# Optimization experiments

Measured on AMD Instinct MI355X. Metric: run time of the kernel, lower is better.

## Reference

```python
import jax, jax.numpy as jnp
import numpy as np

N = 100_000
E = 1_250_000
D = 64
PAIRS = 3  # layer_num=3 -> 3 (SAGE, GIN) pairs
EPS = 1e-5


def _linear_init(key, fi, fo):
    lim = 1.0 / np.sqrt(fi)
    k1, k2 = jax.random.split(key)
    W = jax.random.uniform(k1, (fi, fo), minval=-lim, maxval=lim, dtype=jnp.float32)
    b = jax.random.uniform(k2, (fo,), minval=-lim, maxval=lim, dtype=jnp.float32)
    return W, b


def setup_inputs() -> dict:
    key = jax.random.key(0)
    ks = jax.random.split(key, 40)
    # graph
    src = jax.random.randint(ks[0], (E,), 0, N, dtype=jnp.int32)
    dst = jax.random.randint(ks[1], (E,), 0, N, dtype=jnp.int32)
    sign = (jax.random.randint(ks[2], (E,), 0, 2, dtype=jnp.int32) * 2 - 1)
    edge_index_s = jnp.stack([src, dst, sign], axis=1)  # [E,3]
    init_emb = jax.random.normal(ks[3], (N, D), dtype=jnp.float32)
    rate_b = jax.random.uniform(ks[4], (1,), dtype=jnp.float32)

    def stack_lin(kbase, fi, fo, n):
        Ws, bs = [], []
        for i in range(n):
            W, b = _linear_init(jax.random.fold_in(kbase, i), fi, fo)
            Ws.append(W); bs.append(b)
        return jnp.stack(Ws), jnp.stack(bs)

    sage_lin_W, sage_lin_b = stack_lin(ks[5], D, D, PAIRS)
    sage_norm_w = jnp.ones((PAIRS, D), jnp.float32)
    sage_norm_b = jnp.zeros((PAIRS, D), jnp.float32)
    rsW, rsB = stack_lin(ks[6], 1, D, PAIRS)   # rate_scale Linear(1,D)
    rbW, rbB = stack_lin(ks[7], 1, D, PAIRS)   # rate_bias Linear(1,D)
    sage_rs_w, sage_rs_b = rsW[:, 0, :], rsB   # [PAIRS,D]
    sage_rb_w, sage_rb_b = rbW[:, 0, :], rbB
    gin_W1, gin_b1 = stack_lin(ks[8], D, D, PAIRS)
    gin_W2, gin_b2 = stack_lin(ks[9], D, D, PAIRS)
    fuse_W, fuse_b = _linear_init(ks[10], 2 * PAIRS * D, D)
    ro_W1, ro_b1 = _linear_init(ks[11], D, 128)
    ro_W2, ro_b2 = _linear_init(ks[12], 128, 128)
    ro_W3, ro_b3 = _linear_init(ks[13], 128, 1)
    ro_ln1_g = jnp.ones((128,), jnp.float32); ro_ln1_b = jnp.zeros((128,), jnp.float32)
    ro_ln2_g = jnp.ones((128,), jnp.float32); ro_ln2_b = jnp.zeros((128,), jnp.float32)
    return dict(init_emb=init_emb, edge_index_s=edge_index_s, rate_b=rate_b,
                sage_lin_W=sage_lin_W, sage_lin_b=sage_lin_b,
                sage_norm_w=sage_norm_w, sage_norm_b=sage_norm_b,
                sage_rs_w=sage_rs_w, sage_rs_b=sage_rs_b,
                sage_rb_w=sage_rb_w, sage_rb_b=sage_rb_b,
                gin_W1=gin_W1, gin_b1=gin_b1, gin_W2=gin_W2, gin_b2=gin_b2,
                fuse_W=fuse_W, fuse_b=fuse_b,
                ro_W1=ro_W1, ro_b1=ro_b1, ro_ln1_g=ro_ln1_g, ro_ln1_b=ro_ln1_b,
                ro_W2=ro_W2, ro_b2=ro_b2, ro_ln2_g=ro_ln2_g, ro_ln2_b=ro_ln2_b,
                ro_W3=ro_W3, ro_b3=ro_b3)


def _graph_norm(x, w, b, rs_w, rs_b, rb_w, rb_b, rate):
    # batch stats over nodes (dim 0), biased variance
    mean = x.mean(0, keepdims=True)
    var = x.var(0, keepdims=True)
    x_norm = (x - mean) / jnp.sqrt(var + EPS)
    gamma = w + (rs_w * rate + rs_b)  # rate_scale(rate_b)
    beta = b + (rb_w * rate + rb_b)
    return x_norm * gamma + beta


def _layer_norm(v, g, b):
    m = v.mean(-1, keepdims=True)
    va = v.var(-1, keepdims=True)
    return (v - m) / jnp.sqrt(va + EPS) * g + b


def _forward(init_emb, edge_index_s, rate_b,
             sage_lin_W, sage_lin_b, sage_norm_w, sage_norm_b,
             sage_rs_w, sage_rs_b, sage_rb_w, sage_rb_b,
             gin_W1, gin_b1, gin_W2, gin_b2,
             fuse_W, fuse_b,
             ro_W1, ro_b1, ro_ln1_g, ro_ln1_b,
             ro_W2, ro_b2, ro_ln2_g, ro_ln2_b,
             ro_W3, ro_b3):
    n = init_emb.shape[0]
    src = edge_index_s[:, 0]
    dst = edge_index_s[:, 1]
    sign = edge_index_s[:, 2].astype(init_emb.dtype)
    rate = rate_b.reshape(())
    # degree including self-loop (for mean aggregation with fill_value=1 self loops)
    deg = jax.ops.segment_sum(jnp.ones_like(sign), dst, num_segments=n) + 1.0  # [n]
    gelu = lambda t: jax.nn.gelu(t, approximate=False)  # torch nn.GELU default = exact

    x = init_emb
    outputs = []
    for i in range(PAIRS):
        # --- StableEfficientEdgeSAGEConv (mean aggr, sign-scaled, self-loops, skip=Identity) ---
        xt = x @ sage_lin_W[i] + sage_lin_b[i]
        msg = sign[:, None] * xt[src]                                   # gather + sign scale
        agg = (jax.ops.segment_sum(msg, dst, num_segments=n) + xt) / deg[:, None]
        h = agg + x                                                     # skip (in==out -> Identity)
        h = _graph_norm(h, sage_norm_w[i], sage_norm_b[i],
                        sage_rs_w[i], sage_rs_b[i], sage_rb_w[i], sage_rb_b[i], rate)
        x = gelu(h)                                                     # dropout: eval mode (no-op)
        outputs.append(x)
        # --- GINConv (sum aggr, eps=0, no self-loops) mlp = Lin-GELU-Lin ---
        agg2 = jax.ops.segment_sum(x[src], dst, num_segments=n)
        z = x + agg2
        x = gelu(z @ gin_W1[i] + gin_b1[i]) @ gin_W2[i] + gin_b2[i]
        outputs.append(x)

    x_dense = jnp.concatenate(outputs, axis=1)          # [n, 6*D]
    x_final = x_dense @ fuse_W + fuse_b                 # [n, D]
    # readout MLP (2 hidden layers + head), eval-mode dropout
    hdd = jax.nn.relu(_layer_norm(x_final @ ro_W1 + ro_b1, ro_ln1_g, ro_ln1_b))
    hdd = jax.nn.relu(_layer_norm(hdd @ ro_W2 + ro_b2, ro_ln2_g, ro_ln2_b))
    prob = jax.nn.sigmoid(hdd @ ro_W3 + ro_b3)          # [n, 1]
    return x_final, prob


def reference(init_emb, edge_index_s, rate_b,
              sage_lin_W, sage_lin_b, sage_norm_w, sage_norm_b,
              sage_rs_w, sage_rs_b, sage_rb_w, sage_rb_b,
              gin_W1, gin_b1, gin_W2, gin_b2,
              fuse_W, fuse_b,
              ro_W1, ro_b1, ro_ln1_g, ro_ln1_b,
              ro_W2, ro_b2, ro_ln2_g, ro_ln2_b,
              ro_W3, ro_b3):
    return _forward(init_emb, edge_index_s, rate_b,
                    sage_lin_W, sage_lin_b, sage_norm_w, sage_norm_b,
                    sage_rs_w, sage_rs_b, sage_rb_w, sage_rb_b,
                    gin_W1, gin_b1, gin_W2, gin_b2,
                    fuse_W, fuse_b,
                    ro_W1, ro_b1, ro_ln1_g, ro_ln1_b,
                    ro_W2, ro_b2, ro_ln2_g, ro_ln2_b,
                    ro_W3, ro_b3)
```

## Files before the change

kernel.cpp:

```cpp
#include <hip/hip_runtime.h>
#include <hip/hip_bf16.h>
#include <math.h>


#define NBSHIFT 9
#define NBSIZE  512

__device__ __forceinline__ float gelu_f(float x) {
    return 0.5f * x * (1.0f + erff(x * 0.70710678118654752440f));
}
__device__ __forceinline__ unsigned short f2bf(float x) {
    __hip_bfloat16 h = __float2bfloat16(x);
    return *reinterpret_cast<unsigned short*>(&h);
}
__device__ __forceinline__ unsigned pack2bf(float a, float b) {
    return (unsigned)f2bf(a) | ((unsigned)f2bf(b) << 16);
}
__device__ __forceinline__ float bf2f(unsigned short u) {
    return __uint_as_float((unsigned)u << 16);
}

__global__ __launch_bounds__(256) void gemm64(
    const float* __restrict__ A,
    const float* __restrict__ Wa, const float* __restrict__ ba,
    unsigned short* __restrict__ Cb, int n)
{
    __shared__ __align__(16) float At[64][68];
    __shared__ __align__(16) float Ws[64][68];
    const int tid = threadIdx.x;
    const int tx = tid & 15, ty = tid >> 4;
    const int rowBase = blockIdx.x * 64;

    #pragma unroll
    for (int i = 0; i < 4; ++i) {
        int v  = tid + i * 256;
        int r  = v >> 4;
        int k4 = (v & 15) * 4;
        float4 a = make_float4(0.f, 0.f, 0.f, 0.f);
        int grow = rowBase + r;
        if (grow < n) a = *(const float4*)(A + (size_t)grow * 64 + k4);
        At[k4 + 0][r] = a.x; At[k4 + 1][r] = a.y;
        At[k4 + 2][r] = a.z; At[k4 + 3][r] = a.w;
        *(float4*)&Ws[r][k4] = *(const float4*)(Wa + r * 64 + k4);
    }
    __syncthreads();

    const int r0 = ty * 4, c0 = tx * 4;
    float acc[4][4];
    #pragma unroll
    for (int j = 0; j < 4; ++j) {
        float bv = ba[c0 + j];
        #pragma unroll
        for (int i = 0; i < 4; ++i) acc[i][j] = bv;
    }
    #pragma unroll 16
    for (int k = 0; k < 64; ++k) {
        float4 av = *(const float4*)&At[k][r0];
        float4 wv = *(const float4*)&Ws[k][c0];
        float a4[4] = {av.x, av.y, av.z, av.w};
        float w4[4] = {wv.x, wv.y, wv.z, wv.w};
        #pragma unroll
        for (int i = 0; i < 4; ++i)
            #pragma unroll
            for (int j = 0; j < 4; ++j)
                acc[i][j] = fmaf(a4[i], w4[j], acc[i][j]);
    }
    #pragma unroll
    for (int i = 0; i < 4; ++i) {
        int grow = rowBase + r0 + i;
        if (grow < n) {
            uint2 u;
            u.x = pack2bf(acc[i][0], acc[i][1]);
            u.y = pack2bf(acc[i][2], acc[i][3]);
            *(uint2*)(Cb + (size_t)grow * 64 + c0) = u;
        }
    }
}

template<bool FIRST>
__global__ __launch_bounds__(256) void act_fuse(
    const float* __restrict__ h,
    const float* __restrict__ colsum, const float* __restrict__ colsumsq,
    const float* __restrict__ nw, const float* __restrict__ nb,
    const float* __restrict__ rsw, const float* __restrict__ rsb,
    const float* __restrict__ rbw, const float* __restrict__ rbb,
    const float* __restrict__ rate_p, float inv_n,
    const float* __restrict__ Wf, const float* __restrict__ bf,
    unsigned short* __restrict__ xb, float* __restrict__ xfinal, int n)
{
    __shared__ __align__(16) float At[64][68];
    __shared__ __align__(16) float Ws[64][68];
    __shared__ float ab_s[128];
    const int tid = threadIdx.x;
    const int tx = tid & 15, ty = tid >> 4;
    const int rowBase = blockIdx.x * 64;

    if (tid < 64) {
        float mean = colsum[tid] * inv_n;
        float var  = colsumsq[tid] * inv_n - mean * mean;
        float rstd = rsqrtf(var + 1e-5f);
        float rate = rate_p[0];
        float gamma = nw[tid] + (rsw[tid] * rate + rsb[tid]);
        float beta  = nb[tid] + (rbw[tid] * rate + rbb[tid]);
        float a = rstd * gamma;
        ab_s[tid] = a;
        ab_s[64 + tid] = beta - mean * a;
    }
    __syncthreads();

    #pragma unroll
    for (int i = 0; i < 4; ++i) {
        int v  = tid + i * 256;
        int r  = v >> 4;
        int k4 = (v & 15) * 4;
        int grow = rowBase + r;
        float4 a = make_float4(0.f, 0.f, 0.f, 0.f);
        if (grow < n) {
            float4 hv = *(const float4*)(h + (size_t)grow * 64 + k4);
            a.x = gelu_f(fmaf(hv.x, ab_s[k4 + 0], ab_s[64 + k4 + 0]));
            a.y = gelu_f(fmaf(hv.y, ab_s[k4 + 1], ab_s[64 + k4 + 1]));
            a.z = gelu_f(fmaf(hv.z, ab_s[k4 + 2], ab_s[64 + k4 + 2]));
            a.w = gelu_f(fmaf(hv.w, ab_s[k4 + 3], ab_s[64 + k4 + 3]));
            uint2 u;
            u.x = pack2bf(a.x, a.y);
            u.y = pack2bf(a.z, a.w);
            *(uint2*)(xb + (size_t)grow * 64 + k4) = u;
        }
        At[k4 + 0][r] = a.x; At[k4 + 1][r] = a.y;
        At[k4 + 2][r] = a.z; At[k4 + 3][r] = a.w;
        *(float4*)&Ws[r][k4] = *(const float4*)(Wf + r * 64 + k4);
    }
    __syncthreads();

    const int r0 = ty * 4, c0 = tx * 4;
    float acc[4][4];
    if (FIRST) {
        #pragma unroll
        for (int j = 0; j < 4; ++j) {
            float bv = bf[c0 + j];
            #pragma unroll
            for (int i = 0; i < 4; ++i) acc[i][j] = bv;
        }
    } else {
        #pragma unroll
        for (int i = 0; i < 4; ++i)
            #pragma unroll
            for (int j = 0; j < 4; ++j) acc[i][j] = 0.f;
    }
    #pragma unroll 16
    for (int k = 0; k < 64; ++k) {
        float4 av = *(const float4*)&At[k][r0];
        float4 wv = *(const float4*)&Ws[k][c0];
        float a4[4] = {av.x, av.y, av.z, av.w};
        float w4[4] = {wv.x, wv.y, wv.z, wv.w};
        #pragma unroll
        for (int i = 0; i < 4; ++i)
            #pragma unroll
            for (int j = 0; j < 4; ++j)
                acc[i][j] = fmaf(a4[i], w4[j], acc[i][j]);
    }
    #pragma unroll
    for (int i = 0; i < 4; ++i) {
        int grow = rowBase + r0 + i;
        if (grow < n) {
            float4 r = make_float4(acc[i][0], acc[i][1], acc[i][2], acc[i][3]);
            float* cp = xfinal + (size_t)grow * 64 + c0;
            if (!FIRST) {
                float4 c = *(const float4*)cp;
                r.x += c.x; r.y += c.y; r.z += c.z; r.w += c.w;
            }
            *(float4*)cp = r;
        }
    }
}

template<bool NEXT>
__global__ __launch_bounds__(256) void gin_fuse(
    const float* __restrict__ z,
    const float* __restrict__ W1, const float* __restrict__ b1,
    const float* __restrict__ W2, const float* __restrict__ b2,
    const float* __restrict__ Wf,
    const float* __restrict__ Wn, const float* __restrict__ bn,
    float* __restrict__ xout, float* __restrict__ xfinal,
    unsigned short* __restrict__ bfout, int n)
{
    __shared__ __align__(16) float At[64][68];
    __shared__ __align__(16) float Ws[64][68];
    const int tid = threadIdx.x;
    const int tx = tid & 15, ty = tid >> 4;
    const int rowBase = blockIdx.x * 64;
    const int r0 = ty * 4, c0 = tx * 4;

    #pragma unroll
    for (int i = 0; i < 4; ++i) {
        int v  = tid + i * 256;
        int r  = v >> 4;
        int k4 = (v & 15) * 4;
        float4 a = make_float4(0.f, 0.f, 0.f, 0.f);
        int grow = rowBase + r;
        if (grow < n) a = *(const float4*)(z + (size_t)grow * 64 + k4);
        At[k4 + 0][r] = a.x; At[k4 + 1][r] = a.y;
        At[k4 + 2][r] = a.z; At[k4 + 3][r] = a.w;
        *(float4*)&Ws[r][k4] = *(const float4*)(W1 + r * 64 + k4);
    }
    __syncthreads();

    float acc[4][4];
    #pragma unroll
    for (int j = 0; j < 4; ++j) {
        float bv = b1[c0 + j];
        #pragma unroll
        for (int i = 0; i < 4; ++i) acc[i][j] = bv;
    }
    #pragma unroll 16
    for (int k = 0; k < 64; ++k) {
        float4 av = *(const float4*)&At[k][r0];
        float4 wv = *(const float4*)&Ws[k][c0];
        float a4[4] = {av.x, av.y, av.z, av.w};
        float w4[4] = {wv.x, wv.y, wv.z, wv.w};
        #pragma unroll
        for (int i = 0; i < 4; ++i)
            #pragma unroll
            for (int j = 0; j < 4; ++j)
                acc[i][j] = fmaf(a4[i], w4[j], acc[i][j]);
    }

    __syncthreads();
    #pragma unroll
    for (int i = 0; i < 4; ++i)
        #pragma unroll
        for (int j = 0; j < 4; ++j)
            At[c0 + j][r0 + i] = gelu_f(acc[i][j]);
    #pragma unroll
    for (int i = 0; i < 4; ++i) {
        int v = tid + i * 256;
        int k = v >> 4, c4 = (v & 15) * 4;
        *(float4*)&Ws[k][c4] = *(const float4*)(W2 + k * 64 + c4);
    }
    __syncthreads();
    float acc2[4][4];
    #pragma unroll
    for (int j = 0; j < 4; ++j) {
        float bv = b2[c0 + j];
        #pragma unroll
        for (int i = 0; i < 4; ++i) acc2[i][j] = bv;
    }
    #pragma unroll 16
    for (int k = 0; k < 64; ++k) {
        float4 av = *(const float4*)&At[k][r0];
        float4 wv = *(const float4*)&Ws[k][c0];
        float a4[4] = {av.x, av.y, av.z, av.w};
        float w4[4] = {wv.x, wv.y, wv.z, wv.w};
        #pragma unroll
        for (int i = 0; i < 4; ++i)
            #pragma unroll
            for (int j = 0; j < 4; ++j)
                acc2[i][j] = fmaf(a4[i], w4[j], acc2[i][j]);
    }
    #pragma unroll
    for (int i = 0; i < 4; ++i) {
        int grow = rowBase + r0 + i;
        if (grow < n)
            *(float4*)(xout + (size_t)grow * 64 + c0) =
                make_float4(acc2[i][0], acc2[i][1], acc2[i][2], acc2[i][3]);
    }

    __syncthreads();
    #pragma unroll
    for (int i = 0; i < 4; ++i)
        #pragma unroll
        for (int j = 0; j < 4; ++j)
            At[c0 + j][r0 + i] = acc2[i][j];
    #pragma unroll
    for (int i = 0; i < 4; ++i) {
        int v = tid + i * 256;
        int k = v >> 4, c4 = (v & 15) * 4;
        *(float4*)&Ws[k][c4] = *(const float4*)(Wf + k * 64 + c4);
    }
    __syncthreads();
    float acc3[4][4];
    #pragma unroll
    for (int i = 0; i < 4; ++i)
        #pragma unroll
        for (int j = 0; j < 4; ++j) acc3[i][j] = 0.f;
    #pragma unroll 16
    for (int k = 0; k < 64; ++k) {
        float4 av = *(const float4*)&At[k][r0];
        float4 wv = *(const float4*)&Ws[k][c0];
        float a4[4] = {av.x, av.y, av.z, av.w};
        float w4[4] = {wv.x, wv.y, wv.z, wv.w};
        #pragma unroll
        for (int i = 0; i < 4; ++i)
            #pragma unroll
            for (int j = 0; j < 4; ++j)
                acc3[i][j] = fmaf(a4[i], w4[j], acc3[i][j]);
    }
    #pragma unroll
    for (int i = 0; i < 4; ++i) {
        int grow = rowBase + r0 + i;
        if (grow < n) {
            float* cp = xfinal + (size_t)grow * 64 + c0;
            float4 c = *(const float4*)cp;
            c.x += acc3[i][0]; c.y += acc3[i][1];
            c.z += acc3[i][2]; c.w += acc3[i][3];
            *(float4*)cp = c;
        }
    }

    if (NEXT) {
        __syncthreads();
        #pragma unroll
        for (int i = 0; i < 4; ++i) {
            int v = tid + i * 256;
            int k = v >> 4, c4 = (v & 15) * 4;
            *(float4*)&Ws[k][c4] = *(const float4*)(Wn + k * 64 + c4);
        }
        __syncthreads();
        float acc4[4][4];
        #pragma unroll
        for (int j = 0; j < 4; ++j) {
            float bv = bn[c0 + j];
            #pragma unroll
            for (int i = 0; i < 4; ++i) acc4[i][j] = bv;
        }
        #pragma unroll 16
        for (int k = 0; k < 64; ++k) {
            float4 av = *(const float4*)&At[k][r0];
            float4 wv = *(const float4*)&Ws[k][c0];
            float a4[4] = {av.x, av.y, av.z, av.w};
            float w4[4] = {wv.x, wv.y, wv.z, wv.w};
            #pragma unroll
            for (int i = 0; i < 4; ++i)
                #pragma unroll
                for (int j = 0; j < 4; ++j)
                    acc4[i][j] = fmaf(a4[i], w4[j], acc4[i][j]);
        }
        #pragma unroll
        for (int i = 0; i < 4; ++i) {
            int grow = rowBase + r0 + i;
            if (grow < n) {
                uint2 u;
                u.x = pack2bf(acc4[i][0], acc4[i][1]);
                u.y = pack2bf(acc4[i][2], acc4[i][3]);
                *(uint2*)(bfout + (size_t)grow * 64 + c0) = u;
            }
        }
    }
}

__global__ void init_buckets(int* __restrict__ bucket_cursor, int Bn, int cap) {
    int t = threadIdx.x;
    if (t < Bn) bucket_cursor[t] = t * cap;
}

__global__ __launch_bounds__(256) void bucketA(
    const int* __restrict__ eidx, int* __restrict__ bucket_cursor,
    uint2* __restrict__ inter, int E)
{
    __shared__ int cnt[256], lo[256], cur[256], garr[256];
    __shared__ int tot_s;
    __shared__ uint2 stage[4096];
    const int tid = threadIdx.x;
    cnt[tid] = 0;
    __syncthreads();

    const int base = blockIdx.x * 4096;
    int pay[16], dfull[16];
    #pragma unroll
    for (int i = 0; i < 16; ++i) {
        int e = base + i * 256 + tid;
        dfull[i] = -1;
        if (e < E) {
            int s  = __builtin_nontemporal_load(eidx + e * 3 + 0);
            int d  = __builtin_nontemporal_load(eidx + e * 3 + 1);
            int sg = __builtin_nontemporal_load(eidx + e * 3 + 2);
            if (sg < 0) s |= 0x80000000;
            pay[i] = s;
            dfull[i] = d;
            atomicAdd(&cnt[d >> NBSHIFT], 1);
        }
    }
    __syncthreads();

    lo[tid] = cnt[tid];
    __syncthreads();
    for (int off = 1; off < 256; off <<= 1) {
        int t = (tid >= off) ? lo[tid - off] : 0;
        __syncthreads();
        lo[tid] += t;
        __syncthreads();
    }
    if (tid == 255) tot_s = lo[255];
    int excl = lo[tid] - cnt[tid];
    __syncthreads();
    lo[tid] = excl;
    cur[tid] = 0;
    if (cnt[tid] > 0) garr[tid] = atomicAdd(bucket_cursor + tid, cnt[tid]);
    __syncthreads();

    #pragma unroll
    for (int i = 0; i < 16; ++i) {
        if (dfull[i] >= 0) {
            int k = dfull[i] >> NBSHIFT;
            int r = atomicAdd(&cur[k], 1);
            stage[lo[k] + r] = make_uint2((unsigned)pay[i], (unsigned)dfull[i]);
        }
    }
    __syncthreads();

    const int tot = tot_s;
    for (int i = tid; i < tot; i += 256) {
        uint2 en = stage[i];
        int k = (int)(en.y >> NBSHIFT);
        inter[garr[k] + (i - lo[k])] = en;
    }
}

__global__ __launch_bounds__(256) void bucketB1(
    const uint2* __restrict__ inter, const int* __restrict__ bucket_cursor,
    int* __restrict__ deg_i, int cap, int n)
{
    __shared__ int cnt[NBSIZE];
    const int b = blockIdx.x, tid = threadIdx.x;
    cnt[tid] = 0; cnt[tid + 256] = 0;
    __syncthreads();
    const int base = b * cap;
    const int len = bucket_cursor[b] - base;
    for (int i = tid; i < len; i += 256)
        atomicAdd(&cnt[inter[base + i].y & (NBSIZE - 1)], 1);
    __syncthreads();
    const int nb0 = b << NBSHIFT;
    if (nb0 + tid < n)       deg_i[nb0 + tid]       = cnt[tid];
    if (nb0 + 256 + tid < n) deg_i[nb0 + 256 + tid] = cnt[256 + tid];
}

__global__ __launch_bounds__(256) void bucketB2(
    const uint2* __restrict__ inter, const int* __restrict__ bucket_cursor,
    const int* __restrict__ row_ptr, int* __restrict__ payload, int cap, int n)
{
    __shared__ int cur[NBSIZE];
    const int b = blockIdx.x, tid = threadIdx.x;
    const int nb0 = b << NBSHIFT;
    cur[tid]       = (nb0 + tid < n)       ? row_ptr[nb0 + tid]       : 0;
    cur[tid + 256] = (nb0 + 256 + tid < n) ? row_ptr[nb0 + 256 + tid] : 0;
    __syncthreads();
    const int base = b * cap;
    const int len = bucket_cursor[b] - base;
    for (int i = tid; i < len; i += 256) {
        uint2 en = inter[base + i];
        int pos = atomicAdd(&cur[en.y & (NBSIZE - 1)], 1);
        payload[pos] = (int)en.x;
    }
}

__global__ __launch_bounds__(256) void scan1(
    const int* __restrict__ deg_i, int* __restrict__ blocksum, int n, int chunk)
{
    int b = blockIdx.x;
    int lo = b * chunk, hi = min(lo + chunk, n);
    int s = 0;
    for (int i = lo + (int)threadIdx.x; i < hi; i += 256) s += deg_i[i];
    #pragma unroll
    for (int off = 32; off; off >>= 1) s += __shfl_xor(s, off, 64);
    __shared__ int ws[4];
    if ((threadIdx.x & 63) == 0) ws[threadIdx.x >> 6] = s;
    __syncthreads();
    if (threadIdx.x == 0) blocksum[b] = ws[0] + ws[1] + ws[2] + ws[3];
}

__global__ __launch_bounds__(256) void scan2(
    const int* __restrict__ blocksum, int* __restrict__ blockoff,
    int* __restrict__ row_ptr_n)
{
    int tid = threadIdx.x, lane = tid & 63, wid = tid >> 6;
    int orig = blocksum[tid];
    int v = orig;
    #pragma unroll
    for (int off = 1; off < 64; off <<= 1) {
        int t = __shfl_up(v, off, 64);
        if (lane >= off) v += t;
    }
    __shared__ int wt[4];
    if (lane == 63) wt[wid] = v;
    __syncthreads();
    int woff = 0;
    for (int w = 0; w < wid; ++w) woff += wt[w];
    blockoff[tid] = woff + v - orig;
    if (tid == 255) *row_ptr_n = woff + v;
}

__global__ __launch_bounds__(256) void scan3(
    const int* __restrict__ deg_i, const int* __restrict__ blockoff,
    int* __restrict__ row_ptr, float* __restrict__ rdeg, int n, int chunk)
{
    int b = blockIdx.x;
    int lo = b * chunk, hi = min(lo + chunk, n);
    int carry = blockoff[b];
    int tid = threadIdx.x, lane = tid & 63, wid = tid >> 6;
    __shared__ int wt[4];
    for (int base = lo; base < hi; base += 256) {
        int i = base + tid;
        int orig = (i < hi) ? deg_i[i] : 0;
        int v = orig;
        #pragma unroll
        for (int off = 1; off < 64; off <<= 1) {
            int t = __shfl_up(v, off, 64);
            if (lane >= off) v += t;
        }
        if (lane == 63) wt[wid] = v;
        __syncthreads();
        int woff = 0;
        for (int w = 0; w < wid; ++w) woff += wt[w];
        int tot = wt[0] + wt[1] + wt[2] + wt[3];
        int excl = carry + woff + (v - orig);
        if (i < hi) {
            row_ptr[i] = excl;
            rdeg[i]    = 1.0f / ((float)orig + 1.0f);
        }
        carry += tot;
        __syncthreads();
    }
}

__device__ __forceinline__ void accum8(float* a, uint4 u, float s) {
    a[0] = fmaf(__uint_as_float(u.x << 16),          s, a[0]);
    a[1] = fmaf(__uint_as_float(u.x & 0xffff0000u),  s, a[1]);
    a[2] = fmaf(__uint_as_float(u.y << 16),          s, a[2]);
    a[3] = fmaf(__uint_as_float(u.y & 0xffff0000u),  s, a[3]);
    a[4] = fmaf(__uint_as_float(u.z << 16),          s, a[4]);
    a[5] = fmaf(__uint_as_float(u.z & 0xffff0000u),  s, a[5]);
    a[6] = fmaf(__uint_as_float(u.w << 16),          s, a[6]);
    a[7] = fmaf(__uint_as_float(u.w & 0xffff0000u),  s, a[7]);
}

template<bool SAGE>
__global__ __launch_bounds__(256) void gather64(
    const int* __restrict__ row_ptr, const int* __restrict__ payload,
    const unsigned short* __restrict__ valb, const float* __restrict__ xprev,
    const float* __restrict__ rdeg, float* __restrict__ out,
    float* __restrict__ colsum, float* __restrict__ colsumsq, int n)
{
    const int tid  = threadIdx.x;
    const int lane = tid & 63;
    const int sub  = lane >> 3;
    const int c0   = (lane & 7) * 8;
    const int wid  = tid >> 6;
    int gw = (blockIdx.x * 256 + tid) >> 6;
    int nw = (gridDim.x * 256) >> 6;

    float st[8], st2[8];
    if (SAGE) {
        #pragma unroll
        for (int j = 0; j < 8; ++j) { st[j] = 0.f; st2[j] = 0.f; }
    }

    for (int node = gw; node < n; node += nw) {
        int beg = __builtin_amdgcn_readfirstlane(row_ptr[node]);
        int end = __builtin_amdgcn_readfirstlane(row_ptr[node + 1]);

        float a[8];
        #pragma unroll
        for (int j = 0; j < 8; ++j) a[j] = 0.f;

        int i0 = beg + sub, i1 = beg + 8 + sub;
        bool v0 = i0 < end, v1 = i1 < end;
        int p0 = v0 ? payload[i0] : 0;
        int p1 = v1 ? payload[i1] : 0;

        for (int e = beg; e < end; e += 16) {
            int  q0 = p0,  q1 = p1;
            bool w0 = v0,  w1 = v1;
            int ni0 = e + 16 + sub, ni1 = e + 24 + sub;
            v0 = ni0 < end; v1 = ni1 < end;
            p0 = v0 ? payload[ni0] : 0;
            p1 = v1 ? payload[ni1] : 0;

            int r0 = w0 ? (q0 & 0x7fffffff) : node;
            int r1 = w1 ? (q1 & 0x7fffffff) : node;
            uint4 u0 = *(const uint4*)(valb + (size_t)r0 * 64 + c0);
            uint4 u1 = *(const uint4*)(valb + (size_t)r1 * 64 + c0);
            float s0 = w0 ? ((SAGE && q0 < 0) ? -1.f : 1.f) : 0.f;
            float s1 = w1 ? ((SAGE && q1 < 0) ? -1.f : 1.f) : 0.f;
            accum8(a, u0, s0);
            accum8(a, u1, s1);
        }

        #pragma unroll
        for (int j = 0; j < 8; ++j) {
            a[j] += __shfl_xor(a[j], 8, 64);
            a[j] += __shfl_xor(a[j], 16, 64);
            a[j] += __shfl_xor(a[j], 32, 64);
        }

        if (sub == 0) {
            uint4 us = *(const uint4*)(valb + (size_t)node * 64 + c0);
            a[0] += __uint_as_float(us.x << 16);
            a[1] += __uint_as_float(us.x & 0xffff0000u);
            a[2] += __uint_as_float(us.y << 16);
            a[3] += __uint_as_float(us.y & 0xffff0000u);
            a[4] += __uint_as_float(us.z << 16);
            a[5] += __uint_as_float(us.z & 0xffff0000u);
            a[6] += __uint_as_float(us.w << 16);
            a[7] += __uint_as_float(us.w & 0xffff0000u);
            if (SAGE) {
                float rd = rdeg[node];
                float4 xp0 = *(const float4*)(xprev + (size_t)node * 64 + c0);
                float4 xp1 = *(const float4*)(xprev + (size_t)node * 64 + c0 + 4);
                float xp[8] = {xp0.x, xp0.y, xp0.z, xp0.w,
                               xp1.x, xp1.y, xp1.z, xp1.w};
                #pragma unroll
                for (int j = 0; j < 8; ++j) {
                    float h = fmaf(a[j], rd, xp[j]);
                    st[j]  += h;
                    st2[j] += h * h;
                    a[j] = h;
                }
            }
            *(float4*)(out + (size_t)node * 64 + c0) =
                make_float4(a[0], a[1], a[2], a[3]);
            *(float4*)(out + (size_t)node * 64 + c0 + 4) =
                make_float4(a[4], a[5], a[6], a[7]);
        }
    }

    if (SAGE) {
        __shared__ float sh[2][4][64];
        if (sub == 0) {
            #pragma unroll
            for (int j = 0; j < 8; ++j) {
                sh[0][wid][c0 + j] = st[j];
                sh[1][wid][c0 + j] = st2[j];
            }
        }
        __syncthreads();
        if (tid < 64) {
            float a_ = sh[0][0][tid] + sh[0][1][tid] + sh[0][2][tid] + sh[0][3][tid];
            float b_ = sh[1][0][tid] + sh[1][1][tid] + sh[1][2][tid] + sh[1][3][tid];
            atomicAdd(colsum + tid, a_);
            atomicAdd(colsumsq + tid, b_);
        }
    }
}

__global__ __launch_bounds__(256) void readout1(
    const float* __restrict__ xf, const float* __restrict__ W1,
    const float* __restrict__ b1, const float* __restrict__ g1,
    const float* __restrict__ bt1, float* __restrict__ H, int n)
{
    __shared__ __align__(16) float At[64][68];
    __shared__ __align__(16) float Ws[64][132];
    const int tid = threadIdx.x;
    const int tx = tid & 15, ty = tid >> 4;
    const int rowBase = blockIdx.x * 64;

    #pragma unroll
    for (int i = 0; i < 4; ++i) {
        int v = tid + i * 256;
        int r = v >> 4, k4 = (v & 15) * 4;
        float4 a = make_float4(0.f, 0.f, 0.f, 0.f);
        int grow = rowBase + r;
        if (grow < n) a = *(const float4*)(xf + (size_t)grow * 64 + k4);
        At[k4 + 0][r] = a.x; At[k4 + 1][r] = a.y;
        At[k4 + 2][r] = a.z; At[k4 + 3][r] = a.w;
    }
    #pragma unroll
    for (int i = 0; i < 8; ++i) {
        int v = tid + i * 256;
        int k = v >> 5, c4 = (v & 31) * 4;
        *(float4*)&Ws[k][c4] = *(const float4*)(W1 + k * 128 + c4);
    }
    __syncthreads();

    const int r0 = ty * 4, c0 = tx * 8;
    float acc[4][8];
    #pragma unroll
    for (int j = 0; j < 8; ++j) {
        float bv = b1[c0 + j];
        #pragma unroll
        for (int i = 0; i < 4; ++i) acc[i][j] = bv;
    }
    #pragma unroll 8
    for (int k = 0; k < 64; ++k) {
        float4 av = *(const float4*)&At[k][r0];
        float4 w0 = *(const float4*)&Ws[k][c0];
        float4 w1v = *(const float4*)&Ws[k][c0 + 4];
        float a4[4] = {av.x, av.y, av.z, av.w};
        float w8[8] = {w0.x, w0.y, w0.z, w0.w, w1v.x, w1v.y, w1v.z, w1v.w};
        #pragma unroll
        for (int i = 0; i < 4; ++i)
            #pragma unroll
            for (int j = 0; j < 8; ++j)
                acc[i][j] = fmaf(a4[i], w8[j], acc[i][j]);
    }

    float gj[8], bj[8];
    #pragma unroll
    for (int j = 0; j < 8; ++j) { gj[j] = g1[c0 + j]; bj[j] = bt1[c0 + j]; }
    #pragma unroll
    for (int i = 0; i < 4; ++i) {
        int grow = rowBase + r0 + i;
        float s = 0.f, s2 = 0.f;
        #pragma unroll
        for (int j = 0; j < 8; ++j) { s += acc[i][j]; s2 += acc[i][j] * acc[i][j]; }
        #pragma unroll
        for (int off = 8; off; off >>= 1) {
            s  += __shfl_xor(s, off, 16);
            s2 += __shfl_xor(s2, off, 16);
        }
        float mean = s * (1.f / 128.f);
        float var  = s2 * (1.f / 128.f) - mean * mean;
        float rstd = rsqrtf(var + 1e-5f);
        float o[8];
        #pragma unroll
        for (int j = 0; j < 8; ++j)
            o[j] = fmaxf(fmaf((acc[i][j] - mean) * rstd, gj[j], bj[j]), 0.f);
        if (grow < n) {
            *(float4*)(H + (size_t)grow * 128 + c0)     = make_float4(o[0], o[1], o[2], o[3]);
            *(float4*)(H + (size_t)grow * 128 + c0 + 4) = make_float4(o[4], o[5], o[6], o[7]);
        }
    }
}

__global__ __launch_bounds__(256) void readout2(
    const float* __restrict__ H, const float* __restrict__ W2,
    const float* __restrict__ b2, const float* __restrict__ g2,
    const float* __restrict__ bt2, const float* __restrict__ W3,
    const float* __restrict__ b3, float* __restrict__ prob, int n)
{
    __shared__ __align__(16) float Ht[64][68];
    __shared__ __align__(16) float Ws[64][132];
    const int tid = threadIdx.x;
    const int tx = tid & 15, ty = tid >> 4;
    const int rowBase = blockIdx.x * 64;
    const int r0 = ty * 4, c0 = tx * 8;

    float acc[4][8];
    #pragma unroll
    for (int j = 0; j < 8; ++j) {
        float bv = b2[c0 + j];
        #pragma unroll
        for (int i = 0; i < 4; ++i) acc[i][j] = bv;
    }

    for (int kc = 0; kc < 2; ++kc) {
        if (kc) __syncthreads();
        #pragma unroll
        for (int i = 0; i < 4; ++i) {
            int v = tid + i * 256;
            int r = v >> 4, k4 = (v & 15) * 4;
            float4 a = make_float4(0.f, 0.f, 0.f, 0.f);
            int grow = rowBase + r;
            if (grow < n) a = *(const float4*)(H + (size_t)grow * 128 + kc * 64 + k4);
            Ht[k4 + 0][r] = a.x; Ht[k4 + 1][r] = a.y;
            Ht[k4 + 2][r] = a.z; Ht[k4 + 3][r] = a.w;
        }
        #pragma unroll
        for (int i = 0; i < 8; ++i) {
            int v = tid + i * 256;
            int k = v >> 5, c4 = (v & 31) * 4;
            *(float4*)&Ws[k][c4] = *(const float4*)(W2 + (kc * 64 + k) * 128 + c4);
        }
        __syncthreads();
        #pragma unroll 8
        for (int k = 0; k < 64; ++k) {
            float4 av = *(const float4*)&Ht[k][r0];
            float4 w0 = *(const float4*)&Ws[k][c0];
            float4 w1v = *(const float4*)&Ws[k][c0 + 4];
            float a4[4] = {av.x, av.y, av.z, av.w};
            float w8[8] = {w0.x, w0.y, w0.z, w0.w, w1v.x, w1v.y, w1v.z, w1v.w};
            #pragma unroll
            for (int i = 0; i < 4; ++i)
                #pragma unroll
                for (int j = 0; j < 8; ++j)
                    acc[i][j] = fmaf(a4[i], w8[j], acc[i][j]);
        }
    }

    float gj[8], bj[8], w3[8];
    #pragma unroll
    for (int j = 0; j < 8; ++j) {
        gj[j] = g2[c0 + j]; bj[j] = bt2[c0 + j]; w3[j] = W3[c0 + j];
    }
    const float bias3 = b3[0];
    #pragma unroll
    for (int i = 0; i < 4; ++i) {
        int grow = rowBase + r0 + i;
        float s = 0.f, s2 = 0.f;
        #pragma unroll
        for (int j = 0; j < 8; ++j) { s += acc[i][j]; s2 += acc[i][j] * acc[i][j]; }
        #pragma unroll
        for (int off = 8; off; off >>= 1) {
            s  += __shfl_xor(s, off, 16);
            s2 += __shfl_xor(s2, off, 16);
        }
        float mean = s * (1.f / 128.f);
        float var  = s2 * (1.f / 128.f) - mean * mean;
        float rstd = rsqrtf(var + 1e-5f);
        float d = 0.f;
        #pragma unroll
        for (int j = 0; j < 8; ++j) {
            float v = fmaxf(fmaf((acc[i][j] - mean) * rstd, gj[j], bj[j]), 0.f);
            d = fmaf(v, w3[j], d);
        }
        #pragma unroll
        for (int off = 8; off; off >>= 1) d += __shfl_xor(d, off, 16);
        if (tx == 0 && grow < n)
            prob[grow] = 1.f / (1.f + expf(-(d + bias3)));
    }
}

extern "C" void kernel_launch(void* const* d_in, const int* in_sizes, int n_in,
                              void* d_out, int out_size, void* d_ws, size_t ws_size,
                              hipStream_t stream)
{
    const float* init_emb = (const float*)d_in[0];
    const int*   eidx     = (const int*)d_in[1];
    const float* rate_b   = (const float*)d_in[2];
    const float* sage_W   = (const float*)d_in[3];
    const float* sage_b   = (const float*)d_in[4];
    const float* norm_w   = (const float*)d_in[5];
    const float* norm_b   = (const float*)d_in[6];
    const float* rs_w     = (const float*)d_in[7];
    const float* rs_b     = (const float*)d_in[8];
    const float* rb_w     = (const float*)d_in[9];
    const float* rb_b     = (const float*)d_in[10];
    const float* gin_W1   = (const float*)d_in[11];
    const float* gin_b1   = (const float*)d_in[12];
    const float* gin_W2   = (const float*)d_in[13];
    const float* gin_b2   = (const float*)d_in[14];
    const float* fuse_W   = (const float*)d_in[15];
    const float* fuse_b   = (const float*)d_in[16];
    const float* ro_W1    = (const float*)d_in[17];
    const float* ro_b1    = (const float*)d_in[18];
    const float* ln1_g    = (const float*)d_in[19];
    const float* ln1_b    = (const float*)d_in[20];
    const float* ro_W2    = (const float*)d_in[21];
    const float* ro_b2    = (const float*)d_in[22];
    const float* ln2_g    = (const float*)d_in[23];
    const float* ln2_b    = (const float*)d_in[24];
    const float* ro_W3    = (const float*)d_in[25];
    const float* ro_b3    = (const float*)d_in[26];

    const int N = in_sizes[0] / 64;
    const int E = in_sizes[1] / 3;
    const size_t nf = (size_t)N * 64;

    float* bufA  = (float*)d_ws;
    float* bufB  = bufA + nf;
    float* bufC  = bufB + nf;
    unsigned short* bfbuf = (unsigned short*)(bufC + nf);
    float* rdeg  = (float*)(bfbuf + nf);
    float* stats = rdeg + N;
    int*   row_ptr  = (int*)(stats + 3 * 256);
    int*   deg_i    = row_ptr + (N + 1);
    int*   blocksum = deg_i + N;
    int*   blockoff = blocksum + 256;
    int*   bucket_cursor = blockoff + 256;
    int*   payload  = bucket_cursor + 256;
    uint2* inter    = (uint2*)bufC;

    float* xfinal = (float*)d_out;
    float* prob   = xfinal + nf;
    float* H      = bufA;

    const int gemm_blocks = (N + 63) / 64;
    const int gather_blocks = 2048;
    const int chunk  = (N + 255) / 256;
    const float inv_n = 1.0f / (float)N;

    const int Bn   = (N + NBSIZE - 1) / NBSIZE;
    const int meanb = (E + Bn - 1) / Bn;
    const int cap  = meanb + meanb / 8 + 64;
    const int ablocks = (E + 4095) / 4096;

    hipMemsetAsync(stats, 0, 3 * 256 * sizeof(float), stream);
    init_buckets<<<1, 256, 0, stream>>>(bucket_cursor, Bn, cap);
    bucketA<<<ablocks, 256, 0, stream>>>(eidx, bucket_cursor, inter, E);
    bucketB1<<<Bn, 256, 0, stream>>>(inter, bucket_cursor, deg_i, cap, N);
    scan1<<<256, 256, 0, stream>>>(deg_i, blocksum, N, chunk);
    scan2<<<1, 256, 0, stream>>>(blocksum, blockoff, row_ptr + N);
    scan3<<<256, 256, 0, stream>>>(deg_i, blockoff, row_ptr, rdeg, N, chunk);
    bucketB2<<<Bn, 256, 0, stream>>>(inter, bucket_cursor, row_ptr, payload, cap, N);

    for (int p = 0; p < 3; ++p) {
        const float* Xp = (p == 0) ? init_emb : (p == 1 ? (const float*)bufB : (const float*)bufC);
        float* B2p = (p == 1) ? bufC : bufB;
        float* cs = stats + p * 256;

        if (p == 0)
            gemm64<<<gemm_blocks, 256, 0, stream>>>(
                Xp, sage_W, sage_b, bfbuf, N);
        gather64<true><<<gather_blocks, 256, 0, stream>>>(
            row_ptr, payload, bfbuf, Xp, rdeg, B2p, cs, cs + 64, N);
        if (p == 0)
            act_fuse<true><<<gemm_blocks, 256, 0, stream>>>(
                B2p, cs, cs + 64,
                norm_w + p * 64, norm_b + p * 64, rs_w + p * 64, rs_b + p * 64,
                rb_w + p * 64, rb_b + p * 64, rate_b, inv_n,
                fuse_W, fuse_b, bfbuf, xfinal, N);
        else
            act_fuse<false><<<gemm_blocks, 256, 0, stream>>>(
                B2p, cs, cs + 64,
                norm_w + p * 64, norm_b + p * 64, rs_w + p * 64, rs_b + p * 64,
                rb_w + p * 64, rb_b + p * 64, rate_b, inv_n,
                fuse_W + (2 * p) * 4096, nullptr, bfbuf, xfinal, N);
        gather64<false><<<gather_blocks, 256, 0, stream>>>(
            row_ptr, payload, bfbuf, nullptr, nullptr, B2p, nullptr, nullptr, N);
        if (p < 2)
            gin_fuse<true><<<gemm_blocks, 256, 0, stream>>>(
                B2p, gin_W1 + p * 4096, gin_b1 + p * 64,
                gin_W2 + p * 4096, gin_b2 + p * 64,
                fuse_W + (2 * p + 1) * 4096,
                sage_W + (p + 1) * 4096, sage_b + (p + 1) * 64,
                B2p, xfinal, bfbuf, N);
        else
            gin_fuse<false><<<gemm_blocks, 256, 0, stream>>>(
                B2p, gin_W1 + p * 4096, gin_b1 + p * 64,
                gin_W2 + p * 4096, gin_b2 + p * 64,
                fuse_W + (2 * p + 1) * 4096,
                nullptr, nullptr, B2p, xfinal, nullptr, N);
    }

    readout1<<<gemm_blocks, 256, 0, stream>>>(
        xfinal, ro_W1, ro_b1, ln1_g, ln1_b, H, N);
    readout2<<<gemm_blocks, 256, 0, stream>>>(
        H, ro_W2, ro_b2, ln2_g, ln2_b, ro_W3, ro_b3, prob, N);
}
```

Before: 919.0 us.

## Map one node per 8-lane group in CSR gather instead of one per wavefront

The gather kernel now assigns each node to an 8-lane group, so a wavefront processes 8 nodes at once instead of one. Each group walks its own edge list four edges per iteration, with loop length set by the max degree across the wave. This removes the per-node cross-lane shuffle reduction and the idle lanes on low-degree nodes (average degree is about 12). In exchange, lanes idle when degrees within a wave differ, and column statistics are reduced with shuffles only at the end.

```diff
diff --git a/kernel.cpp b/kernel.cpp
--- a/kernel.cpp
+++ b/kernel.cpp
@@ -542,94 +542,118 @@
 {
     const int tid  = threadIdx.x;
     const int lane = tid & 63;
-    const int sub  = lane >> 3;
-    const int c0   = (lane & 7) * 8;
+    const int j8   = lane & 7;
+    const int c0   = j8 * 8;
     const int wid  = tid >> 6;
-    int gw = (blockIdx.x * 256 + tid) >> 6;
-    int nw = (gridDim.x * 256) >> 6;
+    const int gg0  = (blockIdx.x * 256 + tid) >> 3;
+    const int ng   = (gridDim.x * 256) >> 3;
 
     float st[8], st2[8];
     if (SAGE) {
         #pragma unroll
-        for (int j = 0; j < 8; ++j) { st[j] = 0.f; st2[j] = 0.f; }
-    }
-
-    for (int node = gw; node < n; node += nw) {
-        int beg = __builtin_amdgcn_readfirstlane(row_ptr[node]);
-        int end = __builtin_amdgcn_readfirstlane(row_ptr[node + 1]);
+        for (int k = 0; k < 8; ++k) { st[k] = 0.f; st2[k] = 0.f; }
+    }
+
+    for (int node = gg0; __any(node < n); node += ng) {
+        const bool active  = node < n;
+        const int  selfrow = active ? node : 0;
+        const int  beg     = active ? row_ptr[node]     : 0;
+        const int  end     = active ? row_ptr[node + 1] : 0;
+
+        int t = (end - beg + 3) >> 2;
+        t = max(t, __shfl_xor(t, 8, 64));
+        t = max(t, __shfl_xor(t, 16, 64));
+        t = max(t, __shfl_xor(t, 32, 64));
 
         float a[8];
         #pragma unroll
-        for (int j = 0; j < 8; ++j) a[j] = 0.f;
-
-        int i0 = beg + sub, i1 = beg + 8 + sub;
-        bool v0 = i0 < end, v1 = i1 < end;
-        int p0 = v0 ? payload[i0] : 0;
-        int p1 = v1 ? payload[i1] : 0;
-
-        for (int e = beg; e < end; e += 16) {
-            int  q0 = p0,  q1 = p1;
-            bool w0 = v0,  w1 = v1;
-            int ni0 = e + 16 + sub, ni1 = e + 24 + sub;
-            v0 = ni0 < end; v1 = ni1 < end;
-            p0 = v0 ? payload[ni0] : 0;
-            p1 = v1 ? payload[ni1] : 0;
-
-            int r0 = w0 ? (q0 & 0x7fffffff) : node;
-            int r1 = w1 ? (q1 & 0x7fffffff) : node;
+        for (int k = 0; k < 8; ++k) a[k] = 0.f;
+
+        int p0 = (beg + 0 < end) ? payload[beg + 0] : 0;
+        int p1 = (beg + 1 < end) ? payload[beg + 1] : 0;
+        int p2 = (beg + 2 < end) ? payload[beg + 2] : 0;
+        int p3 = (beg + 3 < end) ? payload[beg + 3] : 0;
+
+        for (int it = 0; it < t; ++it) {
+            const int i0 = beg + (it << 2);
+            const bool w0 = i0 + 0 < end, w1 = i0 + 1 < end;
+            const bool w2 = i0 + 2 < end, w3 = i0 + 3 < end;
+            const int q0 = p0, q1 = p1, q2 = p2, q3 = p3;
+
+            const int r0 = w0 ? (q0 & 0x7fffffff) : selfrow;
+            const int r1 = w1 ? (q1 & 0x7fffffff) : selfrow;
+            const int r2 = w2 ? (q2 & 0x7fffffff) : selfrow;
+            const int r3 = w3 ? (q3 & 0x7fffffff) : selfrow;
             uint4 u0 = *(const uint4*)(valb + (size_t)r0 * 64 + c0);
             uint4 u1 = *(const uint4*)(valb + (size_t)r1 * 64 + c0);
-            float s0 = w0 ? ((SAGE && q0 < 0) ? -1.f : 1.f) : 0.f;
-            float s1 = w1 ? ((SAGE && q1 < 0) ? -1.f : 1.f) : 0.f;
+            uint4 u2 = *(const uint4*)(valb + (size_t)r2 * 64 + c0);
+            uint4 u3 = *(const uint4*)(valb + (size_t)r3 * 64 + c0);
+
+            const int nb = i0 + 4;
+            p0 = (nb + 0 < end) ? payload[nb + 0] : 0;
+            p1 = (nb + 1 < end) ? payload[nb + 1] : 0;
+            p2 = (nb + 2 < end) ? payload[nb + 2] : 0;
+            p3 = (nb + 3 < end) ? payload[nb + 3] : 0;
+
+            const float s0 = w0 ? ((SAGE && q0 < 0) ? -1.f : 1.f) : 0.f;
+            const float s1 = w1 ? ((SAGE && q1 < 0) ? -1.f : 1.f) : 0.f;
+            const float s2 = w2 ? ((SAGE && q2 < 0) ? -1.f : 1.f) : 0.f;
+            const float s3 = w3 ? ((SAGE && q3 < 0) ? -1.f : 1.f) : 0.f;
             accum8(a, u0, s0);
             accum8(a, u1, s1);
-        }
-
-        #pragma unroll
-        for (int j = 0; j < 8; ++j) {
-            a[j] += __shfl_xor(a[j], 8, 64);
-            a[j] += __shfl_xor(a[j], 16, 64);
-            a[j] += __shfl_xor(a[j], 32, 64);
-        }
-
-        if (sub == 0) {
-            uint4 us = *(const uint4*)(valb + (size_t)node * 64 + c0);
-            a[0] += __uint_as_float(us.x << 16);
-            a[1] += __uint_as_float(us.x & 0xffff0000u);
-            a[2] += __uint_as_float(us.y << 16);
-            a[3] += __uint_as_float(us.y & 0xffff0000u);
-            a[4] += __uint_as_float(us.z << 16);
-            a[5] += __uint_as_float(us.z & 0xffff0000u);
-            a[6] += __uint_as_float(us.w << 16);
-            a[7] += __uint_as_float(us.w & 0xffff0000u);
-            if (SAGE) {
-                float rd = rdeg[node];
-                float4 xp0 = *(const float4*)(xprev + (size_t)node * 64 + c0);
-                float4 xp1 = *(const float4*)(xprev + (size_t)node * 64 + c0 + 4);
-                float xp[8] = {xp0.x, xp0.y, xp0.z, xp0.w,
-                               xp1.x, xp1.y, xp1.z, xp1.w};
+            accum8(a, u2, s2);
+            accum8(a, u3, s3);
+        }
+
+        uint4 us = *(const uint4*)(valb + (size_t)selfrow * 64 + c0);
+        accum8(a, us, 1.f);
+
+        if (SAGE) {
+            const float rd = active ? rdeg[node] : 0.f;
+            float4 xp0 = *(const float4*)(xprev + (size_t)selfrow * 64 + c0);
+            float4 xp1 = *(const float4*)(xprev + (size_t)selfrow * 64 + c0 + 4);
+            float xp[8] = {xp0.x, xp0.y, xp0.z, xp0.w,
+                           xp1.x, xp1.y, xp1.z, xp1.w};
+            float h[8];
+            #pragma unroll
+            for (int k = 0; k < 8; ++k) h[k] = fmaf(a[k], rd, xp[k]);
+            if (active) {
                 #pragma unroll
-                for (int j = 0; j < 8; ++j) {
-                    float h = fmaf(a[j], rd, xp[j]);
-                    st[j]  += h;
-                    st2[j] += h * h;
-                    a[j] = h;
+                for (int k = 0; k < 8; ++k) {
+                    st[k]  += h[k];
+                    st2[k] += h[k] * h[k];
                 }
+                *(float4*)(out + (size_t)node * 64 + c0) =
+                    make_float4(h[0], h[1], h[2], h[3]);
+                *(float4*)(out + (size_t)node * 64 + c0 + 4) =
+                    make_float4(h[4], h[5], h[6], h[7]);
             }
-            *(float4*)(out + (size_t)node * 64 + c0) =
-                make_float4(a[0], a[1], a[2], a[3]);
-            *(float4*)(out + (size_t)node * 64 + c0 + 4) =
-                make_float4(a[4], a[5], a[6], a[7]);
+        } else {
+            if (active) {
+                *(float4*)(out + (size_t)node * 64 + c0) =
+                    make_float4(a[0], a[1], a[2], a[3]);
+                *(float4*)(out + (size_t)node * 64 + c0 + 4) =
+                    make_float4(a[4], a[5], a[6], a[7]);
+            }
         }
     }
 
     if (SAGE) {
+        #pragma unroll
+        for (int k = 0; k < 8; ++k) {
+            st[k]  += __shfl_xor(st[k], 8, 64);
+            st[k]  += __shfl_xor(st[k], 16, 64);
+            st[k]  += __shfl_xor(st[k], 32, 64);
+            st2[k] += __shfl_xor(st2[k], 8, 64);
+            st2[k] += __shfl_xor(st2[k], 16, 64);
+            st2[k] += __shfl_xor(st2[k], 32, 64);
+        }
         __shared__ float sh[2][4][64];
-        if (sub == 0) {
-            #pragma unroll
-            for (int j = 0; j < 8; ++j) {
-                sh[0][wid][c0 + j] = st[j];
-                sh[1][wid][c0 + j] = st2[j];
+        if (lane < 8) {
+            #pragma unroll
+            for (int k = 0; k < 8; ++k) {
+                sh[0][wid][c0 + k] = st[k];
+                sh[1][wid][c0 + k] = st2[k];
             }
         }
         __syncthreads();
```

After: 822.7 us. 1.12x faster.
